# Kernel optimization log

Hardware: AMD Instinct MI355X
Metric: run time of the kernel (lower is better)

## Reference

```python
import jax, jax.numpy as jnp
import numpy as np

# Model dims (match init_kwargs)
N, IN_CH, EMB_CH, CONV_CH, NUM_HEAD, ORIG_DIM, DEG = 256, 64, 64, 128, 2, 64, 16
C2 = CONV_CH // 2          # GAT hidden dim
NEG_SLOPE = 0.2            # PyG GATv2 default leaky_relu slope
E_TOTAL = N * DEG + N      # random edges + self loops (add_self_loops=True default)


def setup_inputs() -> dict:
    key = jax.random.key(0)
    ks = jax.random.split(key, 32)

    def p(k, shape):
        # xavier-ish: scale by 1/sqrt(fan_in)
        return jax.random.normal(k, shape, jnp.float32) / np.float32(np.sqrt(shape[0]))

    x = jax.random.normal(ks[0], (N, IN_CH), jnp.float32)
    E_emb = jax.random.normal(ks[1], (N, EMB_CH), jnp.float32)
    # random graph + self loops (PyG GATv2Conv adds self loops by default)
    src = jax.random.randint(ks[2], (N * DEG,), 0, N, jnp.int32)
    dst = jax.random.randint(ks[3], (N * DEG,), 0, N, jnp.int32)
    loops = jnp.arange(N, dtype=jnp.int32)
    edge_index = jnp.stack([jnp.concatenate([src, loops]),
                            jnp.concatenate([dst, loops])])  # [2, E_TOTAL]

    inp = {
        "x": x,
        "E_emb": E_emb,
        "edge_index": edge_index,
        "node_proj": p(ks[4], (IN_CH, CONV_CH)),
        "emb_proj": p(ks[5], (EMB_CH, CONV_CH)),
        # Conv1d(conv_ch, conv_ch, k=2, s=2) on a length-2 signal == two matmuls
        "conv_w0": p(ks[6], (CONV_CH, CONV_CH)),   # applied to E channel (stack pos 0)
        "conv_w1": p(ks[7], (CONV_CH, CONV_CH)),   # applied to masked x (stack pos 1)
        "conv_b": jnp.zeros((CONV_CH,), jnp.float32),
        "lin2_w": p(ks[8], (CONV_CH, C2)),
        "lin2_b": jnp.zeros((C2,), jnp.float32),
        "masked_proj": p(ks[9], (C2, C2)),
        "normal_proj": p(ks[10], (C2, C2)),
        # GATv2 layer 1
        "g1_wl": p(ks[11], (C2, NUM_HEAD * C2)), "g1_bl": jnp.zeros((NUM_HEAD * C2,), jnp.float32),
        "g1_wr": p(ks[12], (C2, NUM_HEAD * C2)), "g1_br": jnp.zeros((NUM_HEAD * C2,), jnp.float32),
        "g1_att": p(ks[13], (NUM_HEAD, C2)), "g1_bias": jnp.zeros((C2,), jnp.float32),
        # GATv2 layer 2
        "g2_wl": p(ks[14], (C2, NUM_HEAD * C2)), "g2_bl": jnp.zeros((NUM_HEAD * C2,), jnp.float32),
        "g2_wr": p(ks[15], (C2, NUM_HEAD * C2)), "g2_br": jnp.zeros((NUM_HEAD * C2,), jnp.float32),
        "g2_att": p(ks[16], (NUM_HEAD, C2)), "g2_bias": jnp.zeros((C2,), jnp.float32),
        "rec_w": p(ks[17], (C2, ORIG_DIM)),
        "rec_b": jnp.zeros((ORIG_DIM,), jnp.float32),
    }
    return inp


def _forward(x, E_emb, edge_index,
             node_proj, emb_proj, conv_w0, conv_w1, conv_b, lin2_w, lin2_b,
             masked_proj, normal_proj,
             g1_wl, g1_bl, g1_wr, g1_br, g1_att, g1_bias,
             g2_wl, g2_bl, g2_wr, g2_br, g2_att, g2_bias,
             rec_w, rec_b):
    n = x.shape[0]
    src, dst = edge_index[0], edge_index[1]

    x_p = x @ node_proj          # [N, CONV_CH]
    E_p = E_emb @ emb_proj       # [N, CONV_CH]
    # conv1d(k=2,s=2) over stacked [E_p, masked_x] -> base is the unmasked result
    x_w1 = x_p @ conv_w1                          # per-row contribution of x
    base = E_p @ conv_w0 + x_w1 + conv_b          # [N, CONV_CH]

    def gatv2(h, wl, bl, wr, br, att, bias):
        # PyG GATv2Conv, concat=False (head mean), negative_slope=0.2, eval mode
        xl = (h @ wl + bl).reshape(n, NUM_HEAD, C2)   # source transform
        xr = (h @ wr + br).reshape(n, NUM_HEAD, C2)   # target transform
        e = jax.nn.leaky_relu(xl[src] + xr[dst], NEG_SLOPE)   # [E, H, C2]
        logit = jnp.einsum('ehc,hc->eh', e, att)              # [E, H]
        mx = jax.ops.segment_max(logit, dst, num_segments=n)  # per-target max
        w = jnp.exp(logit - mx[dst])
        denom = jax.ops.segment_sum(w, dst, num_segments=n)
        alpha = w / (denom[dst] + 1e-16)
        out = jax.ops.segment_sum(xl[src] * alpha[:, :, None], dst, num_segments=n)
        return out.mean(axis=1) + bias                        # [N, C2]

    def per_node(i):
        # masking row i of x_p zeroes its contribution to the conv output
        h = jnp.tanh(base.at[i].add(-x_w1[i]))
        m = h @ lin2_w + lin2_b                               # [N, C2]
        proj = m @ normal_proj
        proj = proj.at[i].set(m[i] @ masked_proj)
        g = jax.nn.elu(gatv2(proj, g1_wl, g1_bl, g1_wr, g1_br, g1_att, g1_bias))
        g = jax.nn.elu(gatv2(g, g2_wl, g2_bl, g2_wr, g2_br, g2_att, g2_bias))
        return g[i] @ rec_w + rec_b                           # only row i is used

    recon = jax.vmap(per_node)(jnp.arange(n))                 # [N, ORIG_DIM]
    return jnp.tanh(recon)


def reference(x, E_emb, edge_index,
              node_proj, emb_proj, conv_w0, conv_w1, conv_b, lin2_w, lin2_b,
              masked_proj, normal_proj,
              g1_wl, g1_bl, g1_wr, g1_br, g1_att, g1_bias,
              g2_wl, g2_bl, g2_wr, g2_br, g2_att, g2_bias,
              rec_w, rec_b):
    return _forward(x, E_emb, edge_index,
                    node_proj, emb_proj, conv_w0, conv_w1, conv_b, lin2_w, lin2_b,
                    masked_proj, normal_proj,
                    g1_wl, g1_bl, g1_wr, g1_br, g1_att, g1_bias,
                    g2_wl, g2_bl, g2_wr, g2_br, g2_att, g2_bias,
                    rec_w, rec_b)
```

## Files before the change

kernel.cpp:

```cpp
#include <hip/hip_runtime.h>
#include <hip/hip_bf16.h>


#define NN 256
#define EDGE_CAP 96
#define E2_CAP 64
#define E_CAP 6144
#define M_CAP 8

#define OFF_X      0
#define OFF_E      16384
#define OFF_NP     32768
#define OFF_EP     40960
#define OFF_CW0    49152
#define OFF_CW1    65536
#define OFF_CB     81920
#define OFF_L2W    82048
#define OFF_L2B    90240
#define OFF_MP     90304
#define OFF_NPJ    94400
#define OFF_G1WL   98496
#define OFF_G1BL   106688
#define OFF_G1WR   106816
#define OFF_G1BR   115008
#define OFF_G1ATT  115136
#define OFF_G1BIAS 115264
#define OFF_G2WL   115328
#define OFF_G2BL   123520
#define OFF_G2WR   123648
#define OFF_G2BR   131840
#define OFF_G2ATT  131968
#define OFF_G2BIAS 132096
#define OFF_RECW   132160
#define OFF_RECB   136256
#define W_TOTAL    136320

__device__ float g_w[W_TOTAL];
__device__ float g_xl0[NN*128], g_xr0[NN*128], g_xlV[NN*128], g_xrV[NN*128];
__device__ float g_xl2_0[NN*128];
__device__ float g_num[NN*128];
__device__ float g_m[NN*2], g_den[NN*2];
__device__ float g_elog[E_CAP*2];
__device__ int   g_in_ptr[NN+1], g_out_ptr[NN+1];
__device__ int   g_in_src[E_CAP], g_out_dst[E_CAP];
__device__ int   g_f32;

__device__ const int c_off[26] = {
  0,16384,32768,40960,49152,65536,81920,82048,90240,90304,94400,98496,
  106688,106816,115008,115136,115264,115328,123520,123648,131840,131968,
  132096,132160,136256,136320};
__device__ const signed char c_seg[44] = {
  0,0,0,0, 1,1,1,1, 2,2, 3,3, 4,4,4,4, 5,5,5,5, 6, 7,7, 8, 9, 10,
  11,11, 12, 13,13, 14, 15, 16, 17,17, 18, 19,19, 20, 21, 22, 23, 24};
__device__ const signed char c_sub[44] = {
  0,1,2,3, 0,1,2,3, 0,1, 0,1, 0,1,2,3, 0,1,2,3, 0, 0,1, 0, 0, 0,
  0,1, 0, 0,1, 0, 0, 0, 0,1, 0, 0,1, 0, 0, 0, 0, 0};

typedef const void* cvp;
__device__ __forceinline__ float b2f(__hip_bfloat16 v) { return __bfloat162float(v); }

__global__ __launch_bounds__(256) void k_init(
    cvp x, cvp E_emb, cvp node_proj, cvp emb_proj,
    cvp conv_w0, cvp conv_w1, cvp conv_b, cvp lin2_w, cvp lin2_b,
    cvp masked_proj, cvp normal_proj,
    cvp g1_wl, cvp g1_bl, cvp g1_wr, cvp g1_br, cvp g1_att, cvp g1_bias,
    cvp g2_wl, cvp g2_bl, cvp g2_wr, cvp g2_br, cvp g2_att, cvp g2_bias,
    cvp rec_w, cvp rec_b,
    int n, const int* __restrict__ ei, int E)
{
  const int t = threadIdx.x, b = blockIdx.x;
  __shared__ int s_cnt;
  if (t == 0) s_cnt = 0;
  __syncthreads();
  {
    const __hip_bfloat16* xb = (const __hip_bfloat16*)x;
    const int lim = n < 4096 ? n : 4096;
    int c = 0;
    for (int i = t; i < lim; i += 256) {
      const float v = b2f(xb[i]);
      if (!(fabsf(v) <= 16.f)) c++;
    }
    if (c) atomicAdd(&s_cnt, c);
  }
  __syncthreads();
  const int f = (s_cnt > 64) ? 1 : 0;

  if (b < 44) {
    cvp segs[25] = {x, E_emb, node_proj, emb_proj, conv_w0, conv_w1, conv_b,
                    lin2_w, lin2_b, masked_proj, normal_proj,
                    g1_wl, g1_bl, g1_wr, g1_br, g1_att, g1_bias,
                    g2_wl, g2_bl, g2_wr, g2_br, g2_att, g2_bias,
                    rec_w, rec_b};
    const int s = c_seg[b];
    cvp p = segs[s];
    const int off = c_off[s];
    const int base = (int)c_sub[b] * 4096;
    int lim = (c_off[s+1] - off) - base;
    if (lim > 4096) lim = 4096;
    if (f) {
      const float* pf = (const float*)p;
      for (int i = t; i < lim; i += 256) g_w[off+base+i] = pf[base+i];
    } else {
      const __hip_bfloat16* pb = (const __hip_bfloat16*)p;
      for (int i = t; i < lim; i += 256) g_w[off+base+i] = b2f(pb[base+i]);
    }
    return;
  }

  __shared__ int cin[NN], cou[NN], pin[NN], pou[NN];
  if (E > E_CAP) E = E_CAP;
  if (t == 0) g_f32 = f;
  cin[t] = 0; cou[t] = 0;
  __syncthreads();
  for (int e = t; e < E; e += 256) {
    atomicAdd(&cin[ei[E+e] & (NN-1)], 1);
    atomicAdd(&cou[ei[e]   & (NN-1)], 1);
  }
  __syncthreads();
  pin[t] = cin[t]; pou[t] = cou[t];
  __syncthreads();
  for (int off = 1; off < NN; off <<= 1) {
    int a = 0, c = 0;
    if (t >= off) { a = pin[t-off]; c = pou[t-off]; }
    __syncthreads();
    if (t >= off) { pin[t] += a; pou[t] += c; }
    __syncthreads();
  }
  const int exi = pin[t] - cin[t];
  const int exo = pou[t] - cou[t];
  g_in_ptr[t] = exi; g_out_ptr[t] = exo;
  if (t == NN-1) { g_in_ptr[NN] = pin[t]; g_out_ptr[NN] = pou[t]; }
  cin[t] = exi; cou[t] = exo;
  __syncthreads();
  for (int e = t; e < E; e += 256) {
    const int s = ei[e] & (NN-1), d = ei[E+e] & (NN-1);
    g_in_src[atomicAdd(&cin[d], 1)] = s;
    g_out_dst[atomicAdd(&cou[s], 1)] = d;
  }
}

__global__ __launch_bounds__(128) void k_dense()
{
  const int j = blockIdx.x, t = threadIdx.x;
  __shared__ float sx[64], sE[64], sxp[128], sEp[128], sh0[128], shm[128],
                   sm0[64], sMm[64], sp0[64], sV[64];
  if (t < 64) { sx[t] = g_w[OFF_X + j*64+t]; sE[t] = g_w[OFF_E + j*64+t]; }
  __syncthreads();
  float a = 0.f, b = 0.f;
  #pragma unroll
  for (int k = 0; k < 64; ++k) {
    a += sx[k] * g_w[OFF_NP + k*128+t];
    b += sE[k] * g_w[OFF_EP + k*128+t];
  }
  sxp[t] = a; sEp[t] = b;
  __syncthreads();
  float xw1 = 0.f, ew0 = 0.f;
  #pragma unroll
  for (int k = 0; k < 128; ++k) {
    xw1 += sxp[k] * g_w[OFF_CW1 + k*128+t];
    ew0 += sEp[k] * g_w[OFF_CW0 + k*128+t];
  }
  const float cb = g_w[OFF_CB + t];
  sh0[t] = tanhf(ew0 + xw1 + cb);
  shm[t] = tanhf(ew0 + cb);
  __syncthreads();
  if (t < 64) {
    float m0 = g_w[OFF_L2B + t], Mm = m0;
    #pragma unroll
    for (int k = 0; k < 128; ++k) {
      const float w = g_w[OFF_L2W + k*64+t];
      m0 += sh0[k]*w; Mm += shm[k]*w;
    }
    sm0[t] = m0; sMm[t] = Mm;
  }
  __syncthreads();
  if (t < 64) {
    float p = 0.f, v = 0.f;
    #pragma unroll
    for (int k = 0; k < 64; ++k) {
      p += sm0[k] * g_w[OFF_NPJ + k*64+t];
      v += sMm[k] * g_w[OFF_MP + k*64+t];
    }
    sp0[t] = p; sV[t] = v;
  }
  __syncthreads();
  float l0 = g_w[OFF_G1BL + t], r0 = g_w[OFF_G1BR + t];
  float lV = l0, rV = r0;
  #pragma unroll
  for (int k = 0; k < 64; ++k) {
    const float wl = g_w[OFF_G1WL + k*128+t], wr = g_w[OFF_G1WR + k*128+t];
    l0 += sp0[k]*wl; r0 += sp0[k]*wr;
    lV += sV[k]*wl;  rV += sV[k]*wr;
  }
  g_xl0[j*128+t] = l0; g_xr0[j*128+t] = r0;
  g_xlV[j*128+t] = lV; g_xrV[j*128+t] = rV;
}

__global__ __launch_bounds__(128) void k_l1base()
{
  const int j = blockIdx.x, t = threadIdx.x;
  __shared__ float sxr[128], satt[128], slog[2][EDGE_CAP], sw[2][EDGE_CAP];
  __shared__ float sinv[2], sg1[64];
  __shared__ int ssrc[EDGE_CAP];
  const int base = g_in_ptr[j];
  int nE = g_in_ptr[j+1] - base;
  if (nE > EDGE_CAP) nE = EDGE_CAP;
  sxr[t] = g_xr0[j*128+t];
  satt[t] = g_w[OFF_G1ATT + t];
  for (int e = t; e < nE; e += 128) ssrc[e] = g_in_src[base+e];
  __syncthreads();
  for (int idx = t; idx < nE*2; idx += 128) {
    const int e = idx >> 1, h = idx & 1, s = ssrc[e];
    const float* xls = g_xl0 + s*128 + h*64;
    float acc = 0.f;
    #pragma unroll
    for (int c = 0; c < 64; ++c) {
      float v = xls[c] + sxr[h*64+c];
      v = v > 0.f ? v : 0.2f*v;
      acc += satt[h*64+c]*v;
    }
    slog[h][e] = acc;
    g_elog[(base+e)*2+h] = acc;
  }
  __syncthreads();
  {
    const int h = t >> 6, lane = t & 63;
    float m = -1e30f;
    for (int e = lane; e < nE; e += 64) m = fmaxf(m, slog[h][e]);
    for (int o = 1; o < 64; o <<= 1) m = fmaxf(m, __shfl_xor(m, o));
    float ssum = 0.f;
    for (int e = lane; e < nE; e += 64) {
      const float w = __expf(slog[h][e]-m); sw[h][e] = w; ssum += w;
    }
    for (int o = 1; o < 64; o <<= 1) ssum += __shfl_xor(ssum, o);
    if (lane == 0) {
      sinv[h] = 1.f/(ssum + 1e-16f);
      g_m[j*2+h] = m; g_den[j*2+h] = ssum;
    }
  }
  __syncthreads();
  if (t < 64) {
    float a0 = 0.f, a1 = 0.f;
    for (int e = 0; e < nE; ++e) {
      const float* xs = g_xl0 + ssrc[e]*128;
      a0 += sw[0][e]*xs[t];
      a1 += sw[1][e]*xs[64+t];
    }
    g_num[j*128+t] = a0; g_num[j*128+64+t] = a1;
    float g = 0.5f*(a0*sinv[0] + a1*sinv[1]) + g_w[OFF_G1BIAS + t];
    g = g > 0.f ? g : expm1f(g);
    sg1[t] = g;
  }
  __syncthreads();
  float acc = g_w[OFF_G2BL + t];
  #pragma unroll
  for (int k = 0; k < 64; ++k) acc += sg1[k]*g_w[OFF_G2WL + k*128+t];
  g_xl2_0[j*128+t] = acc;
}

struct P3s {
  float xl2e[E2_CAP*128];
  float rtmp[M_CAP*128];
  float g1m[M_CAP*64];
  float sgi[64];
  float sxlVi[128], sxl0i[128], sxri[128];
  float satt[128], satt2[128];
  float slog[2][E2_CAP], sw[2][E2_CAP], sinv[2];
  float xr2i[128], sg[64];
  int   slotOf[NN];
  unsigned char isInN[NN];
  int   ssrc2[E2_CAP], listM[M_CAP];
  int   nM;
};

__device__ __forceinline__ void delta_one(P3s& S, int m, int nMl, int i, int t)
{
  if (m >= nMl) return;
  const int lt = t - 128, h = lt >> 6, c = lt & 63;
  const int j = S.listM[m];
  const float mj = g_m[j*2+h];
  float u = S.sxlVi[lt] + g_xr0[j*128+lt];
  u = u > 0.f ? u : 0.2f*u;
  float ln = S.satt[lt]*u;
  for (int o = 1; o < 64; o <<= 1) ln += __shfl_xor(ln, o);
  const float wn1 = __expf(ln - mj);
  const int jb = g_in_ptr[j], jd = g_in_ptr[j+1] - jb;
  float wo = 0.f; int cnt = 0;
  for (int p = c; p < jd; p += 64)
    if (g_in_src[jb+p] == i) { wo += __expf(g_elog[(jb+p)*2+h] - mj); cnt++; }
  for (int o = 1; o < 64; o <<= 1) {
    wo += __shfl_xor(wo, o); cnt += __shfl_xor(cnt, o);
  }
  const float dd = (float)cnt*wn1 - wo;
  const float dn = (float)cnt*wn1*S.sxlVi[lt] - wo*S.sxl0i[lt];
  S.rtmp[m*128+lt] = (g_num[j*128+lt] + dn) / (g_den[j*2+h] + dd + 1e-16f);
}

__global__ __launch_bounds__(256) void k_periter(void* out)
{
  const int i = blockIdx.x, t = threadIdx.x;
  __shared__ P3s S;

  if (t < NN) { S.slotOf[t] = -1; S.isInN[t] = 0; }
  if (t == 0) S.nM = 0;
  if (t < 128) {
    S.satt[t]  = g_w[OFF_G1ATT + t];
    S.satt2[t] = g_w[OFF_G2ATT + t];
    S.sxlVi[t] = g_xlV[i*128+t];
    S.sxl0i[t] = g_xl0[i*128+t];
    S.sxri[t]  = g_xrV[i*128+t];
  }
  __syncthreads();
  if (t == 0) S.slotOf[i] = 0;

  const int b2 = g_in_ptr[i];
  int nE2 = g_in_ptr[i+1] - b2;
  if (nE2 > E2_CAP) nE2 = E2_CAP;
  for (int e = t; e < nE2; e += 256) {
    const int s = g_in_src[b2+e];
    S.ssrc2[e] = s;
    S.isInN[s] = 1;
  }
  __syncthreads();

  const int ob = g_out_ptr[i], onE = g_out_ptr[i+1] - ob;
  for (int e = t; e < onE; e += 256) {
    const int d = g_out_dst[ob+e];
    if (d != i && S.isInN[d]) {
      if (atomicCAS(&S.slotOf[d], -1, -2) == -1) {
        const int p = atomicAdd(&S.nM, 1);
        if (p < M_CAP) { S.listM[p] = d; S.slotOf[d] = p + 1; }
        else S.slotOf[d] = -1;
      }
    }
  }
  for (int idx = t; idx < nE2*2; idx += 256) {
    const int e = idx >> 1, h = idx & 1, s = S.ssrc2[e];
    const float* xls = (s == i) ? (S.sxlVi + h*64) : (g_xl0 + s*128 + h*64);
    float acc = 0.f;
    #pragma unroll
    for (int c = 0; c < 64; ++c) {
      float v = xls[c] + S.sxri[h*64+c];
      v = v > 0.f ? v : 0.2f*v;
      acc += S.satt[h*64+c]*v;
    }
    S.slog[h][e] = acc;
  }
  __syncthreads();
  const int nMl = S.nM > M_CAP ? M_CAP : S.nM;

  if (t < 128) {
    const int h = t >> 6, lane = t & 63;
    float m = -1e30f;
    for (int e = lane; e < nE2; e += 64) m = fmaxf(m, S.slog[h][e]);
    for (int o = 1; o < 64; o <<= 1) m = fmaxf(m, __shfl_xor(m, o));
    float ssum = 0.f;
    for (int e = lane; e < nE2; e += 64) {
      const float w = __expf(S.slog[h][e]-m); S.sw[h][e] = w; ssum += w;
    }
    for (int o = 1; o < 64; o <<= 1) ssum += __shfl_xor(ssum, o);
    if (lane == 0) S.sinv[h] = 1.f/(ssum + 1e-16f);
  } else {
    delta_one(S, 0, nMl, i, t);
  }
  __syncthreads();

  if (t < 64) {
    float a0 = 0.f, a1 = 0.f;
    for (int e = 0; e < nE2; ++e) {
      const int s = S.ssrc2[e];
      const float* xs = (s == i) ? S.sxlVi : (g_xl0 + s*128);
      a0 += S.sw[0][e]*xs[t];
      a1 += S.sw[1][e]*xs[64+t];
    }
    float g = 0.5f*(a0*S.sinv[0] + a1*S.sinv[1]) + g_w[OFF_G1BIAS + t];
    g = g > 0.f ? g : expm1f(g);
    S.sgi[t] = g;
  } else if (t >= 128) {
    delta_one(S, 1, nMl, i, t);
  }
  __syncthreads();

  for (int m = 2; m < nMl; ++m) {
    if (t >= 128) delta_one(S, m, nMl, i, t);
    __syncthreads();
  }

  if (t < 128) {
    float v = g_w[OFF_G2BR + t];
    #pragma unroll
    for (int k = 0; k < 64; ++k) v += S.sgi[k]*g_w[OFF_G2WR + k*128+t];
    S.xr2i[t] = v;
  } else {
    for (int idx = t - 128; idx < nMl*64; idx += 128) {
      const int m = idx >> 6, c = idx & 63;
      float g = 0.5f*(S.rtmp[m*128+c] + S.rtmp[m*128+64+c]) + g_w[OFF_G1BIAS + c];
      g = g > 0.f ? g : expm1f(g);
      S.g1m[m*64+c] = g;
    }
  }
  __syncthreads();

  for (int idx = t; idx < nE2*128; idx += 256) {
    const int e = idx >> 7, c = idx & 127, s = S.ssrc2[e];
    const int sl = S.slotOf[s];
    float v;
    if (sl >= 0) {
      const float* g1r = (sl == 0) ? S.sgi : (S.g1m + (sl-1)*64);
      v = g_w[OFF_G2BL + c];
      #pragma unroll
      for (int k = 0; k < 64; ++k) v += g1r[k]*g_w[OFF_G2WL + k*128+c];
    } else {
      v = g_xl2_0[s*128+c];
    }
    S.xl2e[e*128+c] = v;
  }
  __syncthreads();

  for (int idx = t; idx < nE2*2; idx += 256) {
    const int e = idx >> 1, h = idx & 1;
    const float* xle = S.xl2e + e*128 + h*64;
    float acc = 0.f;
    #pragma unroll
    for (int c = 0; c < 64; ++c) {
      float v = xle[c] + S.xr2i[h*64+c];
      v = v > 0.f ? v : 0.2f*v;
      acc += S.satt2[h*64+c]*v;
    }
    S.slog[h][e] = acc;
  }
  __syncthreads();

  if (t < 128) {
    const int h = t >> 6, lane = t & 63;
    float m = -1e30f;
    for (int e = lane; e < nE2; e += 64) m = fmaxf(m, S.slog[h][e]);
    for (int o = 1; o < 64; o <<= 1) m = fmaxf(m, __shfl_xor(m, o));
    float ssum = 0.f;
    for (int e = lane; e < nE2; e += 64) {
      const float w = __expf(S.slog[h][e]-m); S.sw[h][e] = w; ssum += w;
    }
    for (int o = 1; o < 64; o <<= 1) ssum += __shfl_xor(ssum, o);
    if (lane == 0) S.sinv[h] = 1.f/(ssum + 1e-16f);
  }
  __syncthreads();

  if (t < 64) {
    float a0 = 0.f, a1 = 0.f;
    for (int e = 0; e < nE2; ++e) {
      a0 += S.sw[0][e]*S.xl2e[e*128 + t];
      a1 += S.sw[1][e]*S.xl2e[e*128 + 64 + t];
    }
    float g = 0.5f*(a0*S.sinv[0] + a1*S.sinv[1]) + g_w[OFF_G2BIAS + t];
    g = g > 0.f ? g : expm1f(g);
    S.sg[t] = g;
  }
  __syncthreads();

  if (t < 64) {
    float v = g_w[OFF_RECB + t];
    #pragma unroll
    for (int c = 0; c < 64; ++c) v += S.sg[c]*g_w[OFF_RECW + c*64+t];
    const float r = tanhf(v);
    if (g_f32) ((float*)out)[i*64+t] = r;
    else       ((__hip_bfloat16*)out)[i*64+t] = __float2bfloat16(r);
  }
}

extern "C" void kernel_launch(void* const* d_in, const int* in_sizes, int n_in,
                              void* d_out, int out_size, void* d_ws, size_t ws_size,
                              hipStream_t stream)
{
  const int* ei = (const int*)d_in[2];
  const int E = in_sizes[2] / 2;

  k_init<<<45, 256, 0, stream>>>(
      d_in[0], d_in[1], d_in[3], d_in[4], d_in[5], d_in[6], d_in[7],
      d_in[8], d_in[9], d_in[10], d_in[11], d_in[12], d_in[13], d_in[14],
      d_in[15], d_in[16], d_in[17], d_in[18], d_in[19], d_in[20], d_in[21],
      d_in[22], d_in[23], d_in[24], d_in[25],
      in_sizes[0], ei, E);
  k_dense<<<NN, 128, 0, stream>>>();
  k_l1base<<<NN, 128, 0, stream>>>();
  k_periter<<<NN, 256, 0, stream>>>(d_out);
}
```

Measured before the change: 170.5 us.

## Stage gathered neighbor features in LDS with vectorized loads and skewed indexing

Neighbor rows of xl0 are first copied into shared memory with float4 loads, in both the layer-1 base kernel and the per-node kernel (reusing the xl2e buffer). The attention logit and aggregation loops then read LDS instead of scattered global memory. The inner channel index is rotated by edge id to cut LDS bank conflicts. The l1base kernel moves to 256 threads, and the fp32 weight copy in init uses float4. The trade is extra shared memory (about 48KB in l1base), which lowers occupancy, plus an added barrier.

```diff
diff --git a/kernel.cpp b/kernel.cpp
--- a/kernel.cpp
+++ b/kernel.cpp
@@ -98,8 +98,9 @@
     int lim = (c_off[s+1] - off) - base;
     if (lim > 4096) lim = 4096;
     if (f) {
-      const float* pf = (const float*)p;
-      for (int i = t; i < lim; i += 256) g_w[off+base+i] = pf[base+i];
+      const float4* pf = (const float4*)((const float*)p + base);
+      float4* dst = (float4*)(g_w + off + base);
+      for (int i = t; i < (lim >> 2); i += 256) dst[i] = pf[i];
     } else {
       const __hip_bfloat16* pb = (const __hip_bfloat16*)p;
       for (int i = t; i < lim; i += 256) g_w[off+base+i] = b2f(pb[base+i]);
@@ -196,34 +197,42 @@
   g_xlV[j*128+t] = lV; g_xrV[j*128+t] = rV;
 }
 
-__global__ __launch_bounds__(128) void k_l1base()
+__global__ __launch_bounds__(256) void k_l1base()
 {
   const int j = blockIdx.x, t = threadIdx.x;
-  __shared__ float sxr[128], satt[128], slog[2][EDGE_CAP], sw[2][EDGE_CAP];
-  __shared__ float sinv[2], sg1[64];
+  __shared__ float sxl[EDGE_CAP*128];
+  __shared__ float sxr[128], satt[128];
+  __shared__ float slog[2][EDGE_CAP], sw[2][EDGE_CAP], sinv[2], sg1[64];
   __shared__ int ssrc[EDGE_CAP];
   const int base = g_in_ptr[j];
   int nE = g_in_ptr[j+1] - base;
   if (nE > EDGE_CAP) nE = EDGE_CAP;
-  sxr[t] = g_xr0[j*128+t];
-  satt[t] = g_w[OFF_G1ATT + t];
-  for (int e = t; e < nE; e += 128) ssrc[e] = g_in_src[base+e];
-  __syncthreads();
-  for (int idx = t; idx < nE*2; idx += 128) {
-    const int e = idx >> 1, h = idx & 1, s = ssrc[e];
-    const float* xls = g_xl0 + s*128 + h*64;
+  if (t < 128) { sxr[t] = g_xr0[j*128+t]; satt[t] = g_w[OFF_G1ATT + t]; }
+  for (int e = t; e < nE; e += 256) ssrc[e] = g_in_src[base+e];
+  __syncthreads();
+  for (int idx = t; idx < nE*32; idx += 256) {
+    const int e = idx >> 5, c4 = idx & 31;
+    ((float4*)sxl)[e*32+c4] = ((const float4*)(g_xl0 + ssrc[e]*128))[c4];
+  }
+  __syncthreads();
+  for (int idx = t; idx < nE*2; idx += 256) {
+    const int e = idx >> 1, h = idx & 1;
+    const float* xls = sxl + e*128 + h*64;
+    const float* xr  = sxr + h*64;
+    const float* at  = satt + h*64;
     float acc = 0.f;
     #pragma unroll
     for (int c = 0; c < 64; ++c) {
-      float v = xls[c] + sxr[h*64+c];
+      const int cc = (c + e) & 63;
+      float v = xls[cc] + xr[cc];
       v = v > 0.f ? v : 0.2f*v;
-      acc += satt[h*64+c]*v;
+      acc += at[cc]*v;
     }
     slog[h][e] = acc;
     g_elog[(base+e)*2+h] = acc;
   }
   __syncthreads();
-  {
+  if (t < 128) {
     const int h = t >> 6, lane = t & 63;
     float m = -1e30f;
     for (int e = lane; e < nE; e += 64) m = fmaxf(m, slog[h][e]);
@@ -242,9 +251,8 @@
   if (t < 64) {
     float a0 = 0.f, a1 = 0.f;
     for (int e = 0; e < nE; ++e) {
-      const float* xs = g_xl0 + ssrc[e]*128;
-      a0 += sw[0][e]*xs[t];
-      a1 += sw[1][e]*xs[64+t];
+      a0 += sw[0][e]*sxl[e*128+t];
+      a1 += sw[1][e]*sxl[e*128+64+t];
     }
     g_num[j*128+t] = a0; g_num[j*128+64+t] = a1;
     float g = 0.5f*(a0*sinv[0] + a1*sinv[1]) + g_w[OFF_G1BIAS + t];
@@ -252,10 +260,12 @@
     sg1[t] = g;
   }
   __syncthreads();
-  float acc = g_w[OFF_G2BL + t];
-  #pragma unroll
-  for (int k = 0; k < 64; ++k) acc += sg1[k]*g_w[OFF_G2WL + k*128+t];
-  g_xl2_0[j*128+t] = acc;
+  if (t < 128) {
+    float acc = g_w[OFF_G2BL + t];
+    #pragma unroll
+    for (int k = 0; k < 64; ++k) acc += sg1[k]*g_w[OFF_G2WL + k*128+t];
+    g_xl2_0[j*128+t] = acc;
+  }
 }
 
 struct P3s {
@@ -334,20 +344,31 @@
       }
     }
   }
+  for (int idx = t; idx < nE2*32; idx += 256) {
+    const int e = idx >> 5, c4 = idx & 31, s = S.ssrc2[e];
+    const float4* src = (s == i) ? (const float4*)S.sxlVi
+                                 : (const float4*)(g_xl0 + s*128);
+    ((float4*)S.xl2e)[e*32+c4] = src[c4];
+  }
+  __syncthreads();
+  const int nMl = S.nM > M_CAP ? M_CAP : S.nM;
+
   for (int idx = t; idx < nE2*2; idx += 256) {
-    const int e = idx >> 1, h = idx & 1, s = S.ssrc2[e];
-    const float* xls = (s == i) ? (S.sxlVi + h*64) : (g_xl0 + s*128 + h*64);
+    const int e = idx >> 1, h = idx & 1;
+    const float* xls = S.xl2e + e*128 + h*64;
+    const float* xr  = S.sxri + h*64;
+    const float* at  = S.satt + h*64;
     float acc = 0.f;
     #pragma unroll
     for (int c = 0; c < 64; ++c) {
-      float v = xls[c] + S.sxri[h*64+c];
+      const int cc = (c + e) & 63;
+      float v = xls[cc] + xr[cc];
       v = v > 0.f ? v : 0.2f*v;
-      acc += S.satt[h*64+c]*v;
+      acc += at[cc]*v;
     }
     S.slog[h][e] = acc;
   }
   __syncthreads();
-  const int nMl = S.nM > M_CAP ? M_CAP : S.nM;
 
   if (t < 128) {
     const int h = t >> 6, lane = t & 63;
@@ -368,10 +389,8 @@
   if (t < 64) {
     float a0 = 0.f, a1 = 0.f;
     for (int e = 0; e < nE2; ++e) {
-      const int s = S.ssrc2[e];
-      const float* xs = (s == i) ? S.sxlVi : (g_xl0 + s*128);
-      a0 += S.sw[0][e]*xs[t];
-      a1 += S.sw[1][e]*xs[64+t];
+      a0 += S.sw[0][e]*S.xl2e[e*128 + t];
+      a1 += S.sw[1][e]*S.xl2e[e*128 + 64 + t];
     }
     float g = 0.5f*(a0*S.sinv[0] + a1*S.sinv[1]) + g_w[OFF_G1BIAS + t];
     g = g > 0.f ? g : expm1f(g);
@@ -420,12 +439,15 @@
   for (int idx = t; idx < nE2*2; idx += 256) {
     const int e = idx >> 1, h = idx & 1;
     const float* xle = S.xl2e + e*128 + h*64;
+    const float* xr  = S.xr2i + h*64;
+    const float* at  = S.satt2 + h*64;
     float acc = 0.f;
     #pragma unroll
     for (int c = 0; c < 64; ++c) {
-      float v = xle[c] + S.xr2i[h*64+c];
+      const int cc = (c + e) & 63;
+      float v = xle[cc] + xr[cc];
       v = v > 0.f ? v : 0.2f*v;
-      acc += S.satt2[h*64+c]*v;
+      acc += at[cc]*v;
     }
     S.slog[h][e] = acc;
   }
@@ -481,6 +503,6 @@
       d_in[22], d_in[23], d_in[24], d_in[25],
       in_sizes[0], ei, E);
   k_dense<<<NN, 128, 0, stream>>>();
-  k_l1base<<<NN, 128, 0, stream>>>();
+  k_l1base<<<NN, 256, 0, stream>>>();
   k_periter<<<NN, 256, 0, stream>>>(d_out);
 }
```

New measurement: 175.9 us. 3.2% more time.

## Fuse weight staging and CSR build into dense kernel, read inputs directly

Applied to the files above, without the earlier changes.

Drops the separate init kernel that copied every input into a float staging buffer. The dense kernel now reads weights straight from the original tensors through a templated bf16/f32 loader, and two extra blocks in the same launch build the in- and out-edge CSR, each with a serial scan. This removes one launch and a full copy of the weights, in exchange for bf16 conversion on every weight load and a single-thread prefix sum. The format probe is now done redundantly in every block and checks fewer elements with a lower threshold.

```diff
diff --git a/kernel.cpp b/kernel.cpp
--- a/kernel.cpp
+++ b/kernel.cpp
@@ -8,34 +8,6 @@
 #define E_CAP 6144
 #define M_CAP 8
 
-#define OFF_X      0
-#define OFF_E      16384
-#define OFF_NP     32768
-#define OFF_EP     40960
-#define OFF_CW0    49152
-#define OFF_CW1    65536
-#define OFF_CB     81920
-#define OFF_L2W    82048
-#define OFF_L2B    90240
-#define OFF_MP     90304
-#define OFF_NPJ    94400
-#define OFF_G1WL   98496
-#define OFF_G1BL   106688
-#define OFF_G1WR   106816
-#define OFF_G1BR   115008
-#define OFF_G1ATT  115136
-#define OFF_G1BIAS 115264
-#define OFF_G2WL   115328
-#define OFF_G2BL   123520
-#define OFF_G2WR   123648
-#define OFF_G2BR   131840
-#define OFF_G2ATT  131968
-#define OFF_G2BIAS 132096
-#define OFF_RECW   132160
-#define OFF_RECB   136256
-#define W_TOTAL    136320
-
-__device__ float g_w[W_TOTAL];
 __device__ float g_xl0[NN*128], g_xr0[NN*128], g_xlV[NN*128], g_xrV[NN*128];
 __device__ float g_xl2_0[NN*128];
 __device__ float g_num[NN*128];
@@ -45,196 +17,174 @@
 __device__ int   g_in_src[E_CAP], g_out_dst[E_CAP];
 __device__ int   g_f32;
 
-__device__ const int c_off[26] = {
-  0,16384,32768,40960,49152,65536,81920,82048,90240,90304,94400,98496,
-  106688,106816,115008,115136,115264,115328,123520,123648,131840,131968,
-  132096,132160,136256,136320};
-__device__ const signed char c_seg[44] = {
-  0,0,0,0, 1,1,1,1, 2,2, 3,3, 4,4,4,4, 5,5,5,5, 6, 7,7, 8, 9, 10,
-  11,11, 12, 13,13, 14, 15, 16, 17,17, 18, 19,19, 20, 21, 22, 23, 24};
-__device__ const signed char c_sub[44] = {
-  0,1,2,3, 0,1,2,3, 0,1, 0,1, 0,1,2,3, 0,1,2,3, 0, 0,1, 0, 0, 0,
-  0,1, 0, 0,1, 0, 0, 0, 0,1, 0, 0,1, 0, 0, 0, 0, 0};
-
 typedef const void* cvp;
 __device__ __forceinline__ float b2f(__hip_bfloat16 v) { return __bfloat162float(v); }
 
-__global__ __launch_bounds__(256) void k_init(
-    cvp x, cvp E_emb, cvp node_proj, cvp emb_proj,
-    cvp conv_w0, cvp conv_w1, cvp conv_b, cvp lin2_w, cvp lin2_b,
-    cvp masked_proj, cvp normal_proj,
-    cvp g1_wl, cvp g1_bl, cvp g1_wr, cvp g1_br, cvp g1_att, cvp g1_bias,
-    cvp g2_wl, cvp g2_bl, cvp g2_wr, cvp g2_br, cvp g2_att, cvp g2_bias,
-    cvp rec_w, cvp rec_b,
-    int n, const int* __restrict__ ei, int E)
-{
-  const int t = threadIdx.x, b = blockIdx.x;
-  __shared__ int s_cnt;
-  if (t == 0) s_cnt = 0;
-  __syncthreads();
-  {
-    const __hip_bfloat16* xb = (const __hip_bfloat16*)x;
-    const int lim = n < 4096 ? n : 4096;
-    int c = 0;
-    for (int i = t; i < lim; i += 256) {
-      const float v = b2f(xb[i]);
-      if (!(fabsf(v) <= 16.f)) c++;
-    }
-    if (c) atomicAdd(&s_cnt, c);
-  }
-  __syncthreads();
-  const int f = (s_cnt > 64) ? 1 : 0;
-
-  if (b < 44) {
-    cvp segs[25] = {x, E_emb, node_proj, emb_proj, conv_w0, conv_w1, conv_b,
-                    lin2_w, lin2_b, masked_proj, normal_proj,
-                    g1_wl, g1_bl, g1_wr, g1_br, g1_att, g1_bias,
-                    g2_wl, g2_bl, g2_wr, g2_br, g2_att, g2_bias,
-                    rec_w, rec_b};
-    const int s = c_seg[b];
-    cvp p = segs[s];
-    const int off = c_off[s];
-    const int base = (int)c_sub[b] * 4096;
-    int lim = (c_off[s+1] - off) - base;
-    if (lim > 4096) lim = 4096;
-    if (f) {
-      const float* pf = (const float*)p;
-      for (int i = t; i < lim; i += 256) g_w[off+base+i] = pf[base+i];
-    } else {
-      const __hip_bfloat16* pb = (const __hip_bfloat16*)p;
-      for (int i = t; i < lim; i += 256) g_w[off+base+i] = b2f(pb[base+i]);
-    }
-    return;
-  }
-
-  __shared__ int cin[NN], cou[NN], pin[NN], pou[NN];
-  if (E > E_CAP) E = E_CAP;
-  if (t == 0) g_f32 = f;
-  cin[t] = 0; cou[t] = 0;
-  __syncthreads();
-  for (int e = t; e < E; e += 256) {
-    atomicAdd(&cin[ei[E+e] & (NN-1)], 1);
-    atomicAdd(&cou[ei[e]   & (NN-1)], 1);
-  }
-  __syncthreads();
-  pin[t] = cin[t]; pou[t] = cou[t];
-  __syncthreads();
-  for (int off = 1; off < NN; off <<= 1) {
-    int a = 0, c = 0;
-    if (t >= off) { a = pin[t-off]; c = pou[t-off]; }
-    __syncthreads();
-    if (t >= off) { pin[t] += a; pou[t] += c; }
-    __syncthreads();
-  }
-  const int exi = pin[t] - cin[t];
-  const int exo = pou[t] - cou[t];
-  g_in_ptr[t] = exi; g_out_ptr[t] = exo;
-  if (t == NN-1) { g_in_ptr[NN] = pin[t]; g_out_ptr[NN] = pou[t]; }
-  cin[t] = exi; cou[t] = exo;
-  __syncthreads();
-  for (int e = t; e < E; e += 256) {
-    const int s = ei[e] & (NN-1), d = ei[E+e] & (NN-1);
-    g_in_src[atomicAdd(&cin[d], 1)] = s;
-    g_out_dst[atomicAdd(&cou[s], 1)] = d;
-  }
-}
-
-__global__ __launch_bounds__(128) void k_dense()
-{
-  const int j = blockIdx.x, t = threadIdx.x;
-  __shared__ float sx[64], sE[64], sxp[128], sEp[128], sh0[128], shm[128],
-                   sm0[64], sMm[64], sp0[64], sV[64];
-  if (t < 64) { sx[t] = g_w[OFF_X + j*64+t]; sE[t] = g_w[OFF_E + j*64+t]; }
+template<bool F32>
+__device__ __forceinline__ float LD(cvp p, int i) {
+  if constexpr (F32) return ((const float*)p)[i];
+  else return b2f(((const __hip_bfloat16*)p)[i]);
+}
+
+struct DenseS { float sx[64], sE[64], sxp[128], sEp[128], sh0[128], shm[128],
+                      sm0[64], sMm[64], sp0[64], sV[64]; };
+struct CsrS { int cnt[NN], cur[NN]; };
+
+template<bool F32>
+__device__ __forceinline__ void dense_body(DenseS& S, int j, int t,
+    cvp x, cvp Ee, cvp np_, cvp ep_, cvp cw0, cvp cw1, cvp cb_,
+    cvp l2w, cvp l2b, cvp mp, cvp npj, cvp wl_, cvp bl_, cvp wr_, cvp br_)
+{
+  if (t < 64) { S.sx[t] = LD<F32>(x, j*64+t); S.sE[t] = LD<F32>(Ee, j*64+t); }
   __syncthreads();
   float a = 0.f, b = 0.f;
   #pragma unroll
   for (int k = 0; k < 64; ++k) {
-    a += sx[k] * g_w[OFF_NP + k*128+t];
-    b += sE[k] * g_w[OFF_EP + k*128+t];
-  }
-  sxp[t] = a; sEp[t] = b;
+    a += S.sx[k] * LD<F32>(np_, k*128+t);
+    b += S.sE[k] * LD<F32>(ep_, k*128+t);
+  }
+  S.sxp[t] = a; S.sEp[t] = b;
   __syncthreads();
   float xw1 = 0.f, ew0 = 0.f;
   #pragma unroll
   for (int k = 0; k < 128; ++k) {
-    xw1 += sxp[k] * g_w[OFF_CW1 + k*128+t];
-    ew0 += sEp[k] * g_w[OFF_CW0 + k*128+t];
-  }
-  const float cb = g_w[OFF_CB + t];
-  sh0[t] = tanhf(ew0 + xw1 + cb);
-  shm[t] = tanhf(ew0 + cb);
-  __syncthreads();
-  if (t < 64) {
-    float m0 = g_w[OFF_L2B + t], Mm = m0;
+    xw1 += S.sxp[k] * LD<F32>(cw1, k*128+t);
+    ew0 += S.sEp[k] * LD<F32>(cw0, k*128+t);
+  }
+  const float cb = LD<F32>(cb_, t);
+  S.sh0[t] = tanhf(ew0 + xw1 + cb);
+  S.shm[t] = tanhf(ew0 + cb);
+  __syncthreads();
+  if (t < 64) {
+    float m0 = LD<F32>(l2b, t), Mm = m0;
     #pragma unroll
     for (int k = 0; k < 128; ++k) {
-      const float w = g_w[OFF_L2W + k*64+t];
-      m0 += sh0[k]*w; Mm += shm[k]*w;
-    }
-    sm0[t] = m0; sMm[t] = Mm;
+      const float w = LD<F32>(l2w, k*64+t);
+      m0 += S.sh0[k]*w; Mm += S.shm[k]*w;
+    }
+    S.sm0[t] = m0; S.sMm[t] = Mm;
   }
   __syncthreads();
   if (t < 64) {
     float p = 0.f, v = 0.f;
     #pragma unroll
     for (int k = 0; k < 64; ++k) {
-      p += sm0[k] * g_w[OFF_NPJ + k*64+t];
-      v += sMm[k] * g_w[OFF_MP + k*64+t];
-    }
-    sp0[t] = p; sV[t] = v;
-  }
-  __syncthreads();
-  float l0 = g_w[OFF_G1BL + t], r0 = g_w[OFF_G1BR + t];
+      p += S.sm0[k] * LD<F32>(npj, k*64+t);
+      v += S.sMm[k] * LD<F32>(mp,  k*64+t);
+    }
+    S.sp0[t] = p; S.sV[t] = v;
+  }
+  __syncthreads();
+  float l0 = LD<F32>(bl_, t), r0 = LD<F32>(br_, t);
   float lV = l0, rV = r0;
   #pragma unroll
   for (int k = 0; k < 64; ++k) {
-    const float wl = g_w[OFF_G1WL + k*128+t], wr = g_w[OFF_G1WR + k*128+t];
-    l0 += sp0[k]*wl; r0 += sp0[k]*wr;
-    lV += sV[k]*wl;  rV += sV[k]*wr;
+    const float wl = LD<F32>(wl_, k*128+t), wr = LD<F32>(wr_, k*128+t);
+    l0 += S.sp0[k]*wl; r0 += S.sp0[k]*wr;
+    lV += S.sV[k]*wl;  rV += S.sV[k]*wr;
   }
   g_xl0[j*128+t] = l0; g_xr0[j*128+t] = r0;
   g_xlV[j*128+t] = lV; g_xrV[j*128+t] = rV;
 }
 
-__global__ __launch_bounds__(128) void k_l1base()
-{
-  const int j = blockIdx.x, t = threadIdx.x;
-  __shared__ float sxr[128], satt[128], slog[2][EDGE_CAP], sw[2][EDGE_CAP];
-  __shared__ float sinv[2], sg1[64];
-  __shared__ int ssrc[EDGE_CAP];
+__global__ __launch_bounds__(128) void k_pre(
+    cvp x, cvp Ee, cvp np_, cvp ep_, cvp cw0, cvp cw1, cvp cb_,
+    cvp l2w, cvp l2b, cvp mp, cvp npj, cvp wl_, cvp bl_, cvp wr_, cvp br_,
+    const int* __restrict__ ei, int n, int E)
+{
+  const int t = threadIdx.x, b = blockIdx.x;
+  __shared__ union { DenseS d; CsrS c; } S;
+  __shared__ int s_cnt;
+  if (t == 0) s_cnt = 0;
+  __syncthreads();
+  {
+    const __hip_bfloat16* xb = (const __hip_bfloat16*)x;
+    const int lim = n < 2048 ? n : 2048;
+    int c = 0;
+    for (int i = t; i < lim; i += 128) {
+      const float v = b2f(xb[i]);
+      if (!(fabsf(v) <= 16.f)) c++;
+    }
+    if (c) atomicAdd(&s_cnt, c);
+  }
+  __syncthreads();
+  const int f = (s_cnt > 32) ? 1 : 0;
+  if (E > E_CAP) E = E_CAP;
+
+  if (b < NN) {
+    if (f) dense_body<true >(S.d, b, t, x,Ee,np_,ep_,cw0,cw1,cb_,l2w,l2b,mp,npj,wl_,bl_,wr_,br_);
+    else   dense_body<false>(S.d, b, t, x,Ee,np_,ep_,cw0,cw1,cb_,l2w,l2b,mp,npj,wl_,bl_,wr_,br_);
+    return;
+  }
+
+  const int dir = b - NN;
+  if (dir == 0 && t == 0) g_f32 = f;
+  S.c.cnt[t] = 0; S.c.cnt[t+128] = 0;
+  __syncthreads();
+  for (int e = t; e < E; e += 128) {
+    const int key = (dir == 0) ? (ei[E+e] & (NN-1)) : (ei[e] & (NN-1));
+    atomicAdd(&S.c.cnt[key], 1);
+  }
+  __syncthreads();
+  if (t == 0) {
+    int run = 0;
+    for (int nn = 0; nn < NN; ++nn) { S.c.cur[nn] = run; run += S.c.cnt[nn]; }
+  }
+  __syncthreads();
+  int* gptr = (dir == 0) ? g_in_ptr : g_out_ptr;
+  gptr[t] = S.c.cur[t]; gptr[t+128] = S.c.cur[t+128];
+  if (t == 0) gptr[NN] = E;
+  __syncthreads();
+  for (int e = t; e < E; e += 128) {
+    const int s = ei[e] & (NN-1), d = ei[E+e] & (NN-1);
+    if (dir == 0) g_in_src [atomicAdd(&S.c.cur[d], 1)] = s;
+    else          g_out_dst[atomicAdd(&S.c.cur[s], 1)] = d;
+  }
+}
+
+struct L1S {
+  float sxr[128], satt[128], slog[2][EDGE_CAP], sw[2][EDGE_CAP];
+  float sinv[2], sg1[64];
+  int ssrc[EDGE_CAP];
+};
+
+template<bool F32>
+__device__ __forceinline__ void l1_body(L1S& S, int j, int t,
+    cvp att, cvp bias, cvp g2wl, cvp g2bl)
+{
   const int base = g_in_ptr[j];
   int nE = g_in_ptr[j+1] - base;
   if (nE > EDGE_CAP) nE = EDGE_CAP;
-  sxr[t] = g_xr0[j*128+t];
-  satt[t] = g_w[OFF_G1ATT + t];
-  for (int e = t; e < nE; e += 128) ssrc[e] = g_in_src[base+e];
+  S.sxr[t] = g_xr0[j*128+t];
+  S.satt[t] = LD<F32>(att, t);
+  for (int e = t; e < nE; e += 128) S.ssrc[e] = g_in_src[base+e];
   __syncthreads();
   for (int idx = t; idx < nE*2; idx += 128) {
-    const int e = idx >> 1, h = idx & 1, s = ssrc[e];
+    const int e = idx >> 1, h = idx & 1, s = S.ssrc[e];
     const float* xls = g_xl0 + s*128 + h*64;
     float acc = 0.f;
     #pragma unroll
     for (int c = 0; c < 64; ++c) {
-      float v = xls[c] + sxr[h*64+c];
+      float v = xls[c] + S.sxr[h*64+c];
       v = v > 0.f ? v : 0.2f*v;
-      acc += satt[h*64+c]*v;
-    }
-    slog[h][e] = acc;
+      acc += S.satt[h*64+c]*v;
+    }
+    S.slog[h][e] = acc;
     g_elog[(base+e)*2+h] = acc;
   }
   __syncthreads();
   {
     const int h = t >> 6, lane = t & 63;
     float m = -1e30f;
-    for (int e = lane; e < nE; e += 64) m = fmaxf(m, slog[h][e]);
+    for (int e = lane; e < nE; e += 64) m = fmaxf(m, S.slog[h][e]);
     for (int o = 1; o < 64; o <<= 1) m = fmaxf(m, __shfl_xor(m, o));
     float ssum = 0.f;
     for (int e = lane; e < nE; e += 64) {
-      const float w = __expf(slog[h][e]-m); sw[h][e] = w; ssum += w;
+      const float w = __expf(S.slog[h][e]-m); S.sw[h][e] = w; ssum += w;
     }
     for (int o = 1; o < 64; o <<= 1) ssum += __shfl_xor(ssum, o);
     if (lane == 0) {
-      sinv[h] = 1.f/(ssum + 1e-16f);
+      S.sinv[h] = 1.f/(ssum + 1e-16f);
       g_m[j*2+h] = m; g_den[j*2+h] = ssum;
     }
   }
@@ -242,20 +192,28 @@
   if (t < 64) {
     float a0 = 0.f, a1 = 0.f;
     for (int e = 0; e < nE; ++e) {
-      const float* xs = g_xl0 + ssrc[e]*128;
-      a0 += sw[0][e]*xs[t];
-      a1 += sw[1][e]*xs[64+t];
+      const float* xs = g_xl0 + S.ssrc[e]*128;
+      a0 += S.sw[0][e]*xs[t];
+      a1 += S.sw[1][e]*xs[64+t];
     }
     g_num[j*128+t] = a0; g_num[j*128+64+t] = a1;
-    float g = 0.5f*(a0*sinv[0] + a1*sinv[1]) + g_w[OFF_G1BIAS + t];
+    float g = 0.5f*(a0*S.sinv[0] + a1*S.sinv[1]) + LD<F32>(bias, t);
     g = g > 0.f ? g : expm1f(g);
-    sg1[t] = g;
-  }
-  __syncthreads();
-  float acc = g_w[OFF_G2BL + t];
+    S.sg1[t] = g;
+  }
+  __syncthreads();
+  float acc = LD<F32>(g2bl, t);
   #pragma unroll
-  for (int k = 0; k < 64; ++k) acc += sg1[k]*g_w[OFF_G2WL + k*128+t];
+  for (int k = 0; k < 64; ++k) acc += S.sg1[k]*LD<F32>(g2wl, k*128+t);
   g_xl2_0[j*128+t] = acc;
+}
+
+__global__ __launch_bounds__(128) void k_l1base(cvp att, cvp bias, cvp g2wl, cvp g2bl)
+{
+  __shared__ L1S S;
+  const int f = g_f32;
+  if (f) l1_body<true >(S, blockIdx.x, threadIdx.x, att, bias, g2wl, g2bl);
+  else   l1_body<false>(S, blockIdx.x, threadIdx.x, att, bias, g2wl, g2bl);
 }
 
 struct P3s {
@@ -296,16 +254,16 @@
   S.rtmp[m*128+lt] = (g_num[j*128+lt] + dn) / (g_den[j*2+h] + dd + 1e-16f);
 }
 
-__global__ __launch_bounds__(256) void k_periter(void* out)
-{
-  const int i = blockIdx.x, t = threadIdx.x;
-  __shared__ P3s S;
-
+template<bool F32>
+__device__ __forceinline__ void periter_body(P3s& S, int i, int t,
+    cvp att1, cvp bias1, cvp g2wl, cvp g2bl, cvp g2wr, cvp g2br,
+    cvp att2, cvp bias2, cvp recw, cvp recb, void* out)
+{
   if (t < NN) { S.slotOf[t] = -1; S.isInN[t] = 0; }
   if (t == 0) S.nM = 0;
   if (t < 128) {
-    S.satt[t]  = g_w[OFF_G1ATT + t];
-    S.satt2[t] = g_w[OFF_G2ATT + t];
+    S.satt[t]  = LD<F32>(att1, t);
+    S.satt2[t] = LD<F32>(att2, t);
     S.sxlVi[t] = g_xlV[i*128+t];
     S.sxl0i[t] = g_xl0[i*128+t];
     S.sxri[t]  = g_xrV[i*128+t];
@@ -373,7 +331,7 @@
       a0 += S.sw[0][e]*xs[t];
       a1 += S.sw[1][e]*xs[64+t];
     }
-    float g = 0.5f*(a0*S.sinv[0] + a1*S.sinv[1]) + g_w[OFF_G1BIAS + t];
+    float g = 0.5f*(a0*S.sinv[0] + a1*S.sinv[1]) + LD<F32>(bias1, t);
     g = g > 0.f ? g : expm1f(g);
     S.sgi[t] = g;
   } else if (t >= 128) {
@@ -387,14 +345,14 @@
   }
 
   if (t < 128) {
-    float v = g_w[OFF_G2BR + t];
-    #pragma unroll
-    for (int k = 0; k < 64; ++k) v += S.sgi[k]*g_w[OFF_G2WR + k*128+t];
+    float v = LD<F32>(g2br, t);
+    #pragma unroll
+    for (int k = 0; k < 64; ++k) v += S.sgi[k]*LD<F32>(g2wr, k*128+t);
     S.xr2i[t] = v;
   } else {
     for (int idx = t - 128; idx < nMl*64; idx += 128) {
       const int m = idx >> 6, c = idx & 63;
-      float g = 0.5f*(S.rtmp[m*128+c] + S.rtmp[m*128+64+c]) + g_w[OFF_G1BIAS + c];
+      float g = 0.5f*(S.rtmp[m*128+c] + S.rtmp[m*128+64+c]) + LD<F32>(bias1, c);
       g = g > 0.f ? g : expm1f(g);
       S.g1m[m*64+c] = g;
     }
@@ -407,9 +365,9 @@
     float v;
     if (sl >= 0) {
       const float* g1r = (sl == 0) ? S.sgi : (S.g1m + (sl-1)*64);
-      v = g_w[OFF_G2BL + c];
+      v = LD<F32>(g2bl, c);
       #pragma unroll
-      for (int k = 0; k < 64; ++k) v += g1r[k]*g_w[OFF_G2WL + k*128+c];
+      for (int k = 0; k < 64; ++k) v += g1r[k]*LD<F32>(g2wl, k*128+c);
     } else {
       v = g_xl2_0[s*128+c];
     }
@@ -451,20 +409,32 @@
       a0 += S.sw[0][e]*S.xl2e[e*128 + t];
       a1 += S.sw[1][e]*S.xl2e[e*128 + 64 + t];
     }
-    float g = 0.5f*(a0*S.sinv[0] + a1*S.sinv[1]) + g_w[OFF_G2BIAS + t];
+    float g = 0.5f*(a0*S.sinv[0] + a1*S.sinv[1]) + LD<F32>(bias2, t);
     g = g > 0.f ? g : expm1f(g);
     S.sg[t] = g;
   }
   __syncthreads();
 
   if (t < 64) {
-    float v = g_w[OFF_RECB + t];
-    #pragma unroll
-    for (int c = 0; c < 64; ++c) v += S.sg[c]*g_w[OFF_RECW + c*64+t];
+    float v = LD<F32>(recb, t);
+    #pragma unroll
+    for (int c = 0; c < 64; ++c) v += S.sg[c]*LD<F32>(recw, c*64+t);
     const float r = tanhf(v);
-    if (g_f32) ((float*)out)[i*64+t] = r;
-    else       ((__hip_bfloat16*)out)[i*64+t] = __float2bfloat16(r);
-  }
+    if constexpr (F32) ((float*)out)[i*64+t] = r;
+    else               ((__hip_bfloat16*)out)[i*64+t] = __float2bfloat16(r);
+  }
+}
+
+__global__ __launch_bounds__(256) void k_periter(
+    cvp att1, cvp bias1, cvp g2wl, cvp g2bl, cvp g2wr, cvp g2br,
+    cvp att2, cvp bias2, cvp recw, cvp recb, void* out)
+{
+  __shared__ P3s S;
+  const int f = g_f32;
+  if (f) periter_body<true >(S, blockIdx.x, threadIdx.x,
+      att1, bias1, g2wl, g2bl, g2wr, g2br, att2, bias2, recw, recb, out);
+  else   periter_body<false>(S, blockIdx.x, threadIdx.x,
+      att1, bias1, g2wl, g2bl, g2wr, g2br, att2, bias2, recw, recb, out);
 }
 
 extern "C" void kernel_launch(void* const* d_in, const int* in_sizes, int n_in,
@@ -474,13 +444,11 @@
   const int* ei = (const int*)d_in[2];
   const int E = in_sizes[2] / 2;
 
-  k_init<<<45, 256, 0, stream>>>(
+  k_pre<<<NN+2, 128, 0, stream>>>(
       d_in[0], d_in[1], d_in[3], d_in[4], d_in[5], d_in[6], d_in[7],
       d_in[8], d_in[9], d_in[10], d_in[11], d_in[12], d_in[13], d_in[14],
-      d_in[15], d_in[16], d_in[17], d_in[18], d_in[19], d_in[20], d_in[21],
-      d_in[22], d_in[23], d_in[24], d_in[25],
-      in_sizes[0], ei, E);
-  k_dense<<<NN, 128, 0, stream>>>();
-  k_l1base<<<NN, 128, 0, stream>>>();
-  k_periter<<<NN, 256, 0, stream>>>(d_out);
-}
+      d_in[15], ei, in_sizes[0], E);
+  k_l1base<<<NN, 128, 0, stream>>>(d_in[16], d_in[17], d_in[18], d_in[19]);
+  k_periter<<<NN, 256, 0, stream>>>(d_in[16], d_in[17], d_in[18], d_in[19],
+      d_in[20], d_in[21], d_in[22], d_in[23], d_in[24], d_in[25], d_out);
+}
```

Result: no change. 171.8 us (+0.8%).
